# Kernel tuning notes

Hardware: AMD Instinct MI355X
Metric: run time of the kernel (lower is better)

## Reference

```python
import jax, jax.numpy as jnp
import numpy as np

B, P, ENC, EMB, DEC, ATT, V = 64, 196, 512, 512, 512, 512, 10000
CLS_E, NCLS = 512, 200
MAX_LEN = 52
MAX_T = MAX_LEN - 1  # decode steps = max(caption_lengths) - 1


def setup_inputs() -> dict:
    key = jax.random.key(0)
    ks = jax.random.split(key, 24)
    s = 0.02
    u = lambda k, shp: jax.random.uniform(k, shp, jnp.float32, -0.1, 0.1)
    n = lambda k, shp: jax.random.normal(k, shp, jnp.float32) * s
    cap_len = jax.random.randint(ks[2], (B, 1), 2, MAX_LEN + 1)
    cap_len = cap_len.at[0, 0].set(MAX_LEN)  # ensure max decode length is static MAX_T
    return {
        "encoder_out": jax.random.normal(ks[0], (B, P, ENC), jnp.float32),
        "encoded_captions": jax.random.randint(ks[1], (B, MAX_LEN), 0, V),
        "caption_lengths": cap_len,
        "class_k": jax.random.randint(ks[3], (B, 1), 0, NCLS),
        "emb_W": u(ks[4], (V, EMB)),
        "cls_emb_W": u(ks[5], (NCLS, CLS_E)),
        "enc_att_W": n(ks[6], (ENC, ATT)), "enc_att_b": jnp.zeros((ATT,), jnp.float32),
        "dec_att_W": n(ks[7], (DEC, ATT)), "dec_att_b": jnp.zeros((ATT,), jnp.float32),
        "full_att_w": n(ks[8], (ATT,)), "full_att_b": jnp.zeros((), jnp.float32),
        "init_h_W": n(ks[9], (ENC + CLS_E, DEC)), "init_h_b": jnp.zeros((DEC,), jnp.float32),
        "init_c_W": n(ks[10], (ENC + CLS_E, DEC)), "init_c_b": jnp.zeros((DEC,), jnp.float32),
        "f_beta_W": n(ks[11], (DEC, ENC)), "f_beta_b": jnp.zeros((ENC,), jnp.float32),
        "lstm_Wih": n(ks[12], (4 * DEC, EMB + ENC + CLS_E)),
        "lstm_Whh": n(ks[13], (4 * DEC, DEC)),
        "lstm_bih": jnp.zeros((4 * DEC,), jnp.float32),
        "lstm_bhh": jnp.zeros((4 * DEC,), jnp.float32),
        "fc_W": u(ks[14], (DEC, V)), "fc_b": jnp.zeros((V,), jnp.float32),
    }


def reference(encoder_out, encoded_captions, caption_lengths, class_k,
              emb_W, cls_emb_W, enc_att_W, enc_att_b, dec_att_W, dec_att_b,
              full_att_w, full_att_b, init_h_W, init_h_b, init_c_W, init_c_b,
              f_beta_W, f_beta_b, lstm_Wih, lstm_Whh, lstm_bih, lstm_bhh,
              fc_W, fc_b):
    # Sort by descending caption length (torch: caption_lengths.sort(descending=True))
    lens = caption_lengths[:, 0]
    sort_ind = jnp.argsort(-lens)
    lens_s = lens[sort_ind]
    enc = encoder_out[sort_ind]              # [B,P,ENC]
    caps = encoded_captions[sort_ind]        # [B,L]
    embs = emb_W[caps]                       # [B,L,EMB]
    # NOTE: original code does NOT sort class_k -- faithful to that.
    cls_emb = cls_emb_W[class_k[:, 0]]       # [B,CLS_E] (class_embedding[:,0,:])
    dec_len = lens_s - 1                     # decode_lengths

    init_in = jnp.concatenate([enc.mean(axis=1), cls_emb], axis=1)
    h = init_in @ init_h_W + init_h_b        # [B,DEC]
    c = init_in @ init_c_W + init_c_b
    att1 = enc @ enc_att_W + enc_att_b       # [B,P,ATT] (same every step in torch)

    def step(carry, xs):
        h, c = carry
        emb_t, t = xs                        # emb_t: [B,EMB]
        active = (t < dec_len)[:, None]      # ragged batch_size_t truncation as mask
        # attention
        att2 = h @ dec_att_W + dec_att_b
        e = jnp.einsum('bpa,a->bp', jax.nn.relu(att1 + att2[:, None, :]), full_att_w) + full_att_b
        alpha = jax.nn.softmax(e, axis=1)
        awe = jnp.einsum('bpe,bp->be', enc, alpha)
        gate = jax.nn.sigmoid(h @ f_beta_W + f_beta_b)
        awe = gate * awe
        # LSTMCell (torch gate order: i, f, g, o)
        x = jnp.concatenate([emb_t, awe, cls_emb], axis=1)
        gates = x @ lstm_Wih.T + lstm_bih + h @ lstm_Whh.T + lstm_bhh
        i_, f_, g_, o_ = jnp.split(gates, 4, axis=1)
        c_new = jax.nn.sigmoid(f_) * c + jax.nn.sigmoid(i_) * jnp.tanh(g_)
        h_new = jax.nn.sigmoid(o_) * jnp.tanh(c_new)
        # dropout is inference-mode identity
        pred = jnp.where(active, h_new @ fc_W + fc_b, 0.0)
        h = jnp.where(active, h_new, h)
        c = jnp.where(active, c_new, c)
        return (h, c), pred

    xs = (embs[:, :MAX_T].transpose(1, 0, 2), jnp.arange(MAX_T))
    _, preds = jax.lax.scan(step, (h, c), xs)
    predictions = preds.transpose(1, 0, 2)   # [B,MAX_T,V]
    return predictions, caps, dec_len, sort_ind
```

## Files before the change

### kernel.cpp

```cpp
#include <hip/hip_runtime.h>
#include <cstddef>
#include <cstdint>
#include <math.h>

#define BB 64
#define PP 196
#define ENCD 512
#define DECD 512
#define ATTD 512
#define VOC 10000
#define CLSE 512
#define MAXLEN 52
#define MAXT 51
#define G4 2048
#define XDIM 1536

#define OFF_PRED 0
#define OFF_CAPS (BB * MAXT * VOC)
#define OFF_DECLEN (OFF_CAPS + BB * MAXLEN)
#define OFF_SORT (OFF_DECLEN + BB)

static constexpr size_t W_SORT   = 0;
static constexpr size_t W_DECLEN = 64;
static constexpr size_t W_CAPS   = 128;
static constexpr size_t W_CLS    = 3584;
static constexpr size_t W_H      = W_CLS + BB * CLSE;
static constexpr size_t W_C      = W_H + BB * DECD;
static constexpr size_t W_ININ   = W_C + BB * DECD;
static constexpr size_t W_EXCH   = W_ININ + BB * 1024;
static constexpr size_t W_AWE    = W_EXCH + BB * 1024;
static constexpr size_t W_CLSPRE = W_AWE + BB * ENCD;
static constexpr size_t W_W3P    = W_CLSPRE + BB * G4;
static constexpr size_t W_W2P    = W_W3P + (size_t)256 * 8 * 512;
static constexpr size_t W_HALL   = W_W2P + (size_t)256 * 8 * 1024;
static constexpr size_t W_ATT1   = W_HALL + (size_t)BB * MAXT * DECD;
static constexpr size_t W_CNTP   = W_ATT1 + (size_t)BB * PP * ATTD;
static constexpr size_t W_CNTX   = W_CNTP + 3264;
static constexpr size_t W_PAWE   = W_CNTX + 3264;
static constexpr size_t W_CPRE2  = W_PAWE + (size_t)BB * 4 * 520;
static constexpr size_t W_END    = W_CPRE2 + (size_t)MAXT * BB * G4;

__device__ __forceinline__ float sigm(float x) { return 1.f / (1.f + expf(-x)); }

__device__ __forceinline__ double cohLd(const double* p) {
    return __hip_atomic_load(p, __ATOMIC_RELAXED, __HIP_MEMORY_SCOPE_AGENT);
}
__device__ __forceinline__ float cohLdF(const float* p) {
    return __hip_atomic_load(p, __ATOMIC_RELAXED, __HIP_MEMORY_SCOPE_AGENT);
}
__device__ __forceinline__ void cohSt(double* p, double v) {
    __hip_atomic_store(p, v, __ATOMIC_RELAXED, __HIP_MEMORY_SCOPE_AGENT);
}
__device__ __forceinline__ void cohStF(float* p, float v) {
    __hip_atomic_store(p, v, __ATOMIC_RELAXED, __HIP_MEMORY_SCOPE_AGENT);
}

__global__ void setup_kernel(const int* __restrict__ cap_len, float* __restrict__ out,
                             int* __restrict__ sortind, int* __restrict__ declen,
                             int* __restrict__ cnt) {
    __shared__ int sl[BB];
    int i = threadIdx.x;
    for (int k = i; k < 6528; k += 64) cnt[k] = 0;
    sl[i] = cap_len[i];
    __syncthreads();
    int li = sl[i];
    int rank = 0;
    for (int j = 0; j < BB; j++) {
        int lj = sl[j];
        rank += (lj > li) || (lj == li && j < i);
    }
    sortind[rank] = i;
    declen[rank] = li - 1;
    out[OFF_SORT + rank] = (float)i;
    out[OFF_DECLEN + rank] = (float)(li - 1);
}

__global__ void gather_kernel(const int* __restrict__ ecaps, const int* __restrict__ classk,
                              const float* __restrict__ clsW, const int* __restrict__ sortind,
                              int* __restrict__ caps_i, float* __restrict__ cls,
                              float* __restrict__ out) {
    int idx = blockIdx.x * 256 + threadIdx.x;
    if (idx < BB * MAXLEN) {
        int b = idx / MAXLEN, t2 = idx - b * MAXLEN;
        int sb = sortind[b];
        int v = ecaps[sb * MAXLEN + t2];
// ... 175 lines not shown
            float4 b4 = *(const float4*)&Bs[kk][tx * 4];
            float a[4] = {a4.x, a4.y, a4.z, a4.w};
#pragma unroll
            for (int i = 0; i < 4; i++) {
                acc[i][0] = fmaf(a[i], b4.x, acc[i][0]);
                acc[i][1] = fmaf(a[i], b4.y, acc[i][1]);
                acc[i][2] = fmaf(a[i], b4.z, acc[i][2]);
                acc[i][3] = fmaf(a[i], b4.w, acc[i][3]);
            }
        }
    }
#pragma unroll
    for (int i = 0; i < 4; i++) {
        int bl = ty * 4 + i;
        int n = n0 + tx * 4;
        float4 cp = *(const float4*)&clspreg[bl * G4 + n];
        float4 o;
        o.x = acc[i][0] + cp.x; o.y = acc[i][1] + cp.y;
        o.z = acc[i][2] + cp.z; o.w = acc[i][3] + cp.w;
        *(float4*)&cpre2[((size_t)t * 64 + bl) * G4 + n] = o;
    }
}

__global__ __launch_bounds__(256)
void attq_kernel(const float* __restrict__ att1g, const float* __restrict__ encg,
                 const float* __restrict__ hG, const float* __restrict__ Wd,
                 const float* __restrict__ Fb, const float* __restrict__ dab,
                 const float* __restrict__ fbb, const float* __restrict__ fullw,
                 const float* __restrict__ fullb, const int* __restrict__ sortind,
                 const int* __restrict__ declen, float* __restrict__ exch,
                 float* __restrict__ paweG, int* __restrict__ cntX,
                 int* __restrict__ cntP, float* __restrict__ aweG, int t) {
    const int blk = blockIdx.x;
    const int b = blk & 63, q = blk >> 6;
    if (t >= declen[b]) return;
    const int tid = threadIdx.x;
    const int lane = tid & 63, wvid = tid >> 6;

    __shared__ float hS[512];
    __shared__ float pa[256], pb[256];
    __shared__ float att2F[512];
    __shared__ float esS[52];
    __shared__ float redA[1], redB[1];
    __shared__ float pawe[4 * 520];
    __shared__ int finS;

    hS[tid] = hG[b * 512 + tid];
    hS[tid + 256] = hG[b * 512 + 256 + tid];
    __syncthreads();

    {
        const int c = tid & 127, kh = tid >> 7;
        const int col = 128 * q + c;
        const float* wd = Wd + (size_t)(kh << 8) * 512 + col;
        const float* fb = Fb + (size_t)(kh << 8) * 512 + col;
        const float* hp = hS + (kh << 8);
        float a2 = 0.f, fg = 0.f;
#pragma unroll 16
        for (int k = 0; k < 256; k++) {
            float hv = hp[k];
            a2 = fmaf(hv, wd[(size_t)k * 512], a2);
            fg = fmaf(hv, fb[(size_t)k * 512], fg);
        }
        pa[tid] = a2; pb[tid] = fg;
    }
    __syncthreads();
    if (tid < 128) {
        int col = 128 * q + tid;
        cohStF(&exch[b * 1024 + col], pa[tid] + pa[tid + 128] + dab[col]);
        cohStF(&exch[b * 1024 + 512 + col], pb[tid] + pb[tid + 128] + fbb[col]);
    }
    __syncthreads();
    if (tid == 0) {
        int* cx = &cntX[t * 64 + b];
        __hip_atomic_fetch_add(cx, 1, __ATOMIC_RELAXED, __HIP_MEMORY_SCOPE_AGENT);
        while (__hip_atomic_load(cx, __ATOMIC_RELAXED, __HIP_MEMORY_SCOPE_AGENT) < 4)
            __builtin_amdgcn_s_sleep(2);
    }
    __syncthreads();
    att2F[tid] = cohLdF(&exch[b * 1024 + tid]);
    att2F[tid + 256] = cohLdF(&exch[b * 1024 + 256 + tid]);
    __syncthreads();

    const float fbv = fullb[0];
    {
        float4 t0 = *(const float4*)&att2F[lane * 8];
        float4 t1 = *(const float4*)&att2F[lane * 8 + 4];
        float4 w0 = *(const float4*)&fullw[lane * 8];
        float4 w1 = *(const float4*)&fullw[lane * 8 + 4];
        const float* a1b = att1g + (size_t)b * PP * 512;
        for (int lp = wvid; lp < 49; lp += 4) {
            int p = 49 * q + lp;
            const float4* ar = (const float4*)(a1b + (size_t)p * 512) + lane * 2;
            float4 u0 = ar[0], u1 = ar[1];
            float s = fmaxf(u0.x + t0.x, 0.f) * w0.x + fmaxf(u0.y + t0.y, 0.f) * w0.y
                    + fmaxf(u0.z + t0.z, 0.f) * w0.z + fmaxf(u0.w + t0.w, 0.f) * w0.w
                    + fmaxf(u1.x + t1.x, 0.f) * w1.x + fmaxf(u1.y + t1.y, 0.f) * w1.y
                    + fmaxf(u1.z + t1.z, 0.f) * w1.z + fmaxf(u1.w + t1.w, 0.f) * w1.w;
#pragma unroll
            for (int off = 32; off; off >>= 1) s += __shfl_down(s, off, 64);
            if (lane == 0) esS[lp] = s + fbv;
        }
    }
    __syncthreads();
    if (tid < 64) {
        float v = (tid < 49) ? esS[tid] : -1e30f;
#pragma unroll
        for (int off = 32; off; off >>= 1) v = fmaxf(v, __shfl_down(v, off, 64));
        if (tid == 0) redA[0] = v;
    }
    __syncthreads();
    const float mq = redA[0];
    if (tid < 64) {
        float ev = (tid < 49) ? expf(esS[tid] - mq) : 0.f;
        float sv = ev;
#pragma unroll
        for (int off = 32; off; off >>= 1) sv += __shfl_down(sv, off, 64);
        if (tid == 0) redB[0] = sv;
        if (tid < 49) esS[tid] = ev;
    }
    __syncthreads();
    const float Sq = redB[0];

    const int sb = sortind[b];
    {
        float aw[8] = {};
        const float* encb = encg + (size_t)sb * PP * 512 + lane;
        for (int lp = wvid; lp < 49; lp += 4) {
            int p = 49 * q + lp;
            float al = esS[lp];
            const float* ep = encb + (size_t)p * 512;
#pragma unroll
            for (int i = 0; i < 8; i++) aw[i] = fmaf(al, ep[i << 6], aw[i]);
        }
#pragma unroll
        for (int i = 0; i < 8; i++) pawe[wvid * 520 + (i << 6) + lane] = aw[i];
    }
    __syncthreads();
    {
        const int k2 = 2 * tid;
        const int base = ((b << 2) + q) * 520;
        float s0 = pawe[k2] + pawe[520 + k2] + pawe[2 * 520 + k2] + pawe[3 * 520 + k2];
        float s1 = pawe[k2 + 1] + pawe[520 + k2 + 1] + pawe[2 * 520 + k2 + 1] + pawe[3 * 520 + k2 + 1];
        double d;
        *(float2*)&d = make_float2(s0, s1);
        cohSt((double*)&paweG[base + k2], d);
        if (tid == 0) {
            cohStF(&paweG[base + 512], Sq);
            cohStF(&paweG[base + 513], mq);
        }
    }
    __syncthreads();

    if (tid == 0) {
        int prev = __hip_atomic_fetch_add(&cntP[t * 64 + b], 1,
                                          __ATOMIC_RELAXED, __HIP_MEMORY_SCOPE_AGENT);
        finS = (prev == 3);
    }
    __syncthreads();
    if (finS) {
        float mv[4], sv[4];
#pragma unroll
        for (int qq = 0; qq < 4; qq++) {
            mv[qq] = cohLdF(&paweG[((b << 2) + qq) * 520 + 513]);
            sv[qq] = cohLdF(&paweG[((b << 2) + qq) * 520 + 512]);
        }
        float M = fmaxf(fmaxf(mv[0], mv[1]), fmaxf(mv[2], mv[3]));
        float f0 = expf(mv[0] - M), f1 = expf(mv[1] - M);
        float f2 = expf(mv[2] - M), f3 = expf(mv[3] - M);
        float inv = 1.f / (sv[0] * f0 + sv[1] * f1 + sv[2] * f2 + sv[3] * f3);
        const int k2 = 2 * tid;
        const double* pd = (const double*)paweG;
        float a0, a1;
        {
            double d0 = cohLd(pd + ((b << 2) + 0) * 260 + tid);
            double d1 = cohLd(pd + ((b << 2) + 1) * 260 + tid);
            double d2 = cohLd(pd + ((b << 2) + 2) * 260 + tid);
            double d3 = cohLd(pd + ((b << 2) + 3) * 260 + tid);
            float2 g0 = *(float2*)&d0, g1 = *(float2*)&d1;
            float2 g2 = *(float2*)&d2, g3 = *(float2*)&d3;
            a0 = g0.x * f0 + g1.x * f1 + g2.x * f2 + g3.x * f3;
            a1 = g0.y * f0 + g1.y * f1 + g2.y * f2 + g3.y * f3;
        }
        double gpair = cohLd((const double*)&exch[b * 1024 + 512 + k2]);
        float2 g2v = *(float2*)&gpair;
        float2 o = make_float2(a0 * inv * sigm(g2v.x), a1 * inv * sigm(g2v.y));
        *(float2*)&aweG[b * 512 + k2] = o;
    }
}

template<int PRE>
__global__ __launch_bounds__(256)
void gatestep_kernel(const float* __restrict__ embW, const float* __restrict__ W2p,
                     const float* __restrict__ W3p, const float* __restrict__ cpre,
                     const float* __restrict__ aweG, const float* __restrict__ hG,
                     const int* __restrict__ caps_i, const int* __restrict__ declen,
                     float* __restrict__ hOut, float* __restrict__ cG,
                     float* __restrict__ hall, int t) {
    const int j = blockIdx.x, tid = threadIdx.x;
    const int lane = tid & 63, wvid = tid >> 6;
    const int d0 = j * 2;
    const int NCH = PRE ? 8 : 12;
    const int WST = PRE ? 516 : 1028;
    __shared__ float stage[64 * 132];
    __shared__ float W2res[8 * 1028];
    __shared__ float W3res[8 * 516];
    __shared__ float Gs[8 * 66];
    __shared__ float CsS[64 * 8];
    __shared__ int capS[64];
    __shared__ int declen_s[64];

    if (PRE) {
        for (int idx = tid; idx < 1024; idx += 256) {
            int cc = idx >> 7, pos = (idx & 127) << 2;
            *(float4*)&W2res[cc * 516 + pos] =
                *(const float4*)&W2p[(size_t)j * 8192 + cc * 1024 + 512 + pos];
        }
    } else {
        for (int idx = tid; idx < 2048; idx += 256) {
            int cc = idx >> 8, pos = (idx & 255) << 2;
            *(float4*)&W2res[cc * 1028 + pos] =
                *(const float4*)&W2p[(size_t)j * 8192 + cc * 1024 + pos];
        }
    }
    for (int idx = tid; idx < 1024; idx += 256) {
        int cc = idx >> 7, pos = (idx & 127) << 2;
        *(float4*)&W3res[cc * 516 + pos] =
            *(const float4*)&W3p[(size_t)j * 4096 + cc * 512 + pos];
    }
    for (int idx = tid; idx < 512; idx += 256) {
        int r = idx >> 3, cc = idx & 7;
        CsS[idx] = cpre[(r << 11) + ((cc >> 1) << 9) + d0 + (cc & 1)];
    }
    if (tid < 64) {
        if (!PRE) capS[tid] = caps_i[tid * MAXLEN + t];
        declen_s[tid] = declen[tid];
    }

    float ac0 = 0.f, ac1 = 0.f;
    for (int ch = 0; ch < NCH; ch++) {
        __syncthreads();
        {
            const float4* src;
            if (PRE) {
                src = (ch < 4)
                    ? (const float4*)(aweG + ((size_t)lane << 9) + (ch << 7) + (wvid << 5))
                    : (const float4*)(hG + ((size_t)lane << 9) + ((ch - 4) << 7) + (wvid << 5));
            } else {
                if (ch < 4)
                    src = (const float4*)(embW + ((size_t)capS[lane] << 9) + (ch << 7) + (wvid << 5));
                else if (ch < 8)
                    src = (const float4*)(aweG + ((size_t)lane << 9) + ((ch - 4) << 7) + (wvid << 5));
                else
                    src = (const float4*)(hG + ((size_t)lane << 9) + ((ch - 8) << 7) + (wvid << 5));
            }
            float4 tmp[8];
#pragma unroll
            for (int i = 0; i < 8; i++) tmp[i] = src[i];
#pragma unroll
            for (int i = 0; i < 8; i++)
                *(float4*)&stage[lane * 132 + (wvid << 5) + (i << 2)] = tmp[i];
        }
        __syncthreads();
        const float* sp = &stage[lane * 132];
        const int hh0 = PRE ? 4 : 8;
        const float* v0p = (ch < hh0) ? &W2res[wvid * WST + (ch << 7)]
                                      : &W3res[wvid * 516 + ((ch - hh0) << 7)];
        const float* v1p = (ch < hh0) ? &W2res[(wvid + 4) * WST + (ch << 7)]
                                      : &W3res[(wvid + 4) * 516 + ((ch - hh0) << 7)];
#pragma unroll 8
        for (int kk = 0; kk < 128; kk += 4) {
            float4 av = *(const float4*)(sp + kk);
            float4 u0 = *(const float4*)(v0p + kk);
            float4 u1 = *(const float4*)(v1p + kk);
            ac0 = fmaf(av.x, u0.x, fmaf(av.y, u0.y, fmaf(av.z, u0.z, fmaf(av.w, u0.w, ac0))));
            ac1 = fmaf(av.x, u1.x, fmaf(av.y, u1.y, fmaf(av.z, u1.z, fmaf(av.w, u1.w, ac1))));
        }
    }
    Gs[wvid * 66 + lane]       = ac0 + CsS[(lane << 3) + wvid];
    Gs[(wvid + 4) * 66 + lane] = ac1 + CsS[(lane << 3) + wvid + 4];
    __syncthreads();
    if (tid < 128) {
        int r2 = tid & 63, dd = tid >> 6;
        if (t < declen_s[r2]) {
            float iv = Gs[(0 + dd) * 66 + r2];
            float fv = Gs[(2 + dd) * 66 + r2];
            float gv = Gs[(4 + dd) * 66 + r2];
            float ov = Gs[(6 + dd) * 66 + r2];
            float cold = cG[r2 * 512 + d0 + dd];
            float cn = sigm(fv) * cold + sigm(iv) * tanhf(gv);
            float hn = sigm(ov) * tanhf(cn);
            cG[r2 * 512 + d0 + dd] = cn;
            hOut[r2 * 512 + d0 + dd] = hn;
            hall[((size_t)r2 * MAXT + t) * 512 + d0 + dd] = hn;
        }
    }
}

__global__ __launch_bounds__(256)
void fc_kernel(const float* __restrict__ hall, const float* __restrict__ fcW,
               const float* __restrict__ fcb, const int* __restrict__ declen,
               float* __restrict__ out) {
    __shared__ float As[16][68];
    __shared__ float Bs[16][132];
    int tid = threadIdx.x;
    int n0 = blockIdx.x * 128, m0 = blockIdx.y * 64;
    int tx = tid & 15, ty = tid >> 4;
    int lm = tid >> 2, lk4 = (tid & 3) * 4;
    int bkk = tid >> 4, bnn8 = (tid & 15) * 8;
    const float* arow = hall + (size_t)(m0 + lm) * DECD;
    bool nfull = (n0 + 128 <= VOC);
    float acc[4][8] = {};
    for (int k0 = 0; k0 < 512; k0 += 16) {
        float4 av = *(const float4*)(arow + k0 + lk4);
        float4 bv0, bv1;
        const float* bp = fcW + (size_t)(k0 + bkk) * VOC;
        if (nfull) {
            bv0 = *(const float4*)(bp + n0 + bnn8);
            bv1 = *(const float4*)(bp + n0 + bnn8 + 4);
        } else {
            int nb = n0 + bnn8;
            float tv[8];
#pragma unroll
            for (int u = 0; u < 8; u++) tv[u] = (nb + u < VOC) ? bp[nb + u] : 0.f;
            bv0 = make_float4(tv[0], tv[1], tv[2], tv[3]);
            bv1 = make_float4(tv[4], tv[5], tv[6], tv[7]);
        }
        __syncthreads();
        As[lk4 + 0][lm] = av.x; As[lk4 + 1][lm] = av.y;
        As[lk4 + 2][lm] = av.z; As[lk4 + 3][lm] = av.w;
        *(float4*)&Bs[bkk][bnn8] = bv0;
        *(float4*)&Bs[bkk][bnn8 + 4] = bv1;
        __syncthreads();
#pragma unroll
        for (int kk = 0; kk < 16; kk++) {
            float4 a4 = *(const float4*)&As[kk][ty * 4];
            float4 b40 = *(const float4*)&Bs[kk][tx * 8];
            float4 b41 = *(const float4*)&Bs[kk][tx * 8 + 4];
            float a[4] = {a4.x, a4.y, a4.z, a4.w};
#pragma unroll
            for (int i = 0; i < 4; i++) {
                acc[i][0] = fmaf(a[i], b40.x, acc[i][0]);
                acc[i][1] = fmaf(a[i], b40.y, acc[i][1]);
                acc[i][2] = fmaf(a[i], b40.z, acc[i][2]);
                acc[i][3] = fmaf(a[i], b40.w, acc[i][3]);
                acc[i][4] = fmaf(a[i], b41.x, acc[i][4]);
                acc[i][5] = fmaf(a[i], b41.y, acc[i][5]);
                acc[i][6] = fmaf(a[i], b41.z, acc[i][6]);
                acc[i][7] = fmaf(a[i], b41.w, acc[i][7]);
            }
        }
    }
#pragma unroll
    for (int i = 0; i < 4; i++) {
        int m = m0 + ty * 4 + i;
        int b = m / MAXT, tq = m - b * MAXT;
        bool act = tq < declen[b];
        int n = n0 + tx * 8;
        if (nfull) {
            float4 o0, o1;
            o0.x = act ? acc[i][0] + fcb[n + 0] : 0.f;
            o0.y = act ? acc[i][1] + fcb[n + 1] : 0.f;
            o0.z = act ? acc[i][2] + fcb[n + 2] : 0.f;
            o0.w = act ? acc[i][3] + fcb[n + 3] : 0.f;
            o1.x = act ? acc[i][4] + fcb[n + 4] : 0.f;
            o1.y = act ? acc[i][5] + fcb[n + 5] : 0.f;
            o1.z = act ? acc[i][6] + fcb[n + 6] : 0.f;
            o1.w = act ? acc[i][7] + fcb[n + 7] : 0.f;
            *(float4*)(out + (size_t)m * VOC + n) = o0;
            *(float4*)(out + (size_t)m * VOC + n + 4) = o1;
        } else {
#pragma unroll
            for (int jj = 0; jj < 8; jj++) {
                int nn = n + jj;
                if (nn < VOC) out[(size_t)m * VOC + nn] = act ? acc[i][jj] + fcb[nn] : 0.f;
            }
        }
    }
}

extern "C" void kernel_launch(void* const* d_in, const int* in_sizes, int n_in,
                              void* d_out, int out_size, void* d_ws, size_t ws_size,
                              hipStream_t stream) {
    const float* enc     = (const float*)d_in[0];
    const int*   ecaps   = (const int*)d_in[1];
    const int*   lens    = (const int*)d_in[2];
    const int*   classk  = (const int*)d_in[3];
    const float* embW    = (const float*)d_in[4];
    const float* clsW    = (const float*)d_in[5];
    const float* encattW = (const float*)d_in[6];
    const float* encattb = (const float*)d_in[7];
    const float* decattW = (const float*)d_in[8];
    const float* decattb = (const float*)d_in[9];
    const float* fullw   = (const float*)d_in[10];
    const float* fullb   = (const float*)d_in[11];
    const float* ihW     = (const float*)d_in[12];
    const float* ihb     = (const float*)d_in[13];
    const float* icW     = (const float*)d_in[14];
    const float* icb     = (const float*)d_in[15];
    const float* fbW     = (const float*)d_in[16];
    const float* fbb     = (const float*)d_in[17];
    const float* Wih     = (const float*)d_in[18];
    const float* Whh     = (const float*)d_in[19];
    const float* bih     = (const float*)d_in[20];
    const float* bhh     = (const float*)d_in[21];
    const float* fcW     = (const float*)d_in[22];
    const float* fcb     = (const float*)d_in[23];

    float* out = (float*)d_out;
    float* ws  = (float*)d_ws;
    int*   wsi = (int*)d_ws;

    int*   sortind = wsi + W_SORT;
    int*   declen  = wsi + W_DECLEN;
    int*   caps_i  = wsi + W_CAPS;
    float* cls     = ws + W_CLS;
    float* h       = ws + W_H;
    float* c       = ws + W_C;
    float* initin  = ws + W_ININ;
    float* exch    = ws + W_EXCH;
    float* awe     = ws + W_AWE;
    float* clspre  = ws + W_CLSPRE;
    float* W3p     = ws + W_W3P;
    float* W2p     = ws + W_W2P;
    float* hall    = ws + W_HALL;
    float* att1    = ws + W_ATT1;
    int*   cntP    = wsi + W_CNTP;
    int*   cntX    = wsi + W_CNTX;
    float* pawe    = ws + W_PAWE;
    float* cpre2   = ws + W_CPRE2;

    const bool pre = ws_size >= W_END * 4;

    setup_kernel<<<1, 64, 0, stream>>>(lens, out, sortind, declen, cntP);
    gather_kernel<<<141, 256, 0, stream>>>(ecaps, classk, clsW, sortind, caps_i, cls, out);
    mean_cls_kernel<<<BB, 256, 0, stream>>>(enc, cls, sortind, initin);
    init_hc_kernel<<<256, 256, 0, stream>>>(initin, ihW, ihb, icW, icb, h, c);
    pack_w2p_kernel<<<8192, 256, 0, stream>>>(Wih, W2p);
    pack_w3p_kernel<<<4096, 256, 0, stream>>>(Whh, W3p);
    att1_kernel<<<dim3(8, 196), 256, 0, stream>>>(enc, encattW, encattb, sortind, att1);
    clspre_kernel<<<32, 256, 0, stream>>>(cls, Wih, bih, bhh, clspre);
    if (pre)
        embpre_kernel<<<dim3(32, 51), 256, 0, stream>>>(embW, Wih, clspre, caps_i, cpre2);

    for (int t = 0; t < MAXT; t++) {
        attq_kernel<<<256, 256, 0, stream>>>(att1, enc, h, decattW, fbW,
                                             decattb, fbb, fullw, fullb,
                                             sortind, declen, exch, pawe,
                                             cntX, cntP, awe, t);
        if (pre)
            gatestep_kernel<1><<<256, 256, 0, stream>>>(embW, W2p, W3p,
                cpre2 + (size_t)t * 64 * G4, awe, h, caps_i, declen, h, c, hall, t);
        else
            gatestep_kernel<0><<<256, 256, 0, stream>>>(embW, W2p, W3p,
                clspre, awe, h, caps_i, declen, h, c, hall, t);
    }

    fc_kernel<<<dim3(79, 51), 256, 0, stream>>>(hall, fcW, fcb, declen, out);
}
```

Before: 3.720 ms.

## Fuse decode loop into one persistent cooperative kernel with flag-based sync

Replaces the 102 per-step kernel launches (attention plus gate step per timestep) with a single cooperative persistent kernel that loops over all timesteps. Blocks coordinate through global flags for awe readiness and per-block h completion, with h double-buffered. Weight slices stay resident in shared memory across steps, so they are not reloaded every step. The fc kernel's per-thread column mapping is also changed to split into two strided halves. The cost is larger shared memory per block and spin-wait synchronization, with deadlock risk if all 256 blocks cannot be co-resident.

```diff
diff --git a/kernel.cpp b/kernel.cpp
--- a/kernel.cpp
+++ b/kernel.cpp
@@ -1,4 +1,5 @@
 #include <hip/hip_runtime.h>
+#include <hip/hip_cooperative_groups.h>
 #include <cstddef>
 #include <cstdint>
 #include <math.h>
@@ -23,9 +24,14 @@
 static constexpr size_t W_SORT   = 0;
 static constexpr size_t W_DECLEN = 64;
 static constexpr size_t W_CAPS   = 128;
-static constexpr size_t W_CLS    = 3584;
+static constexpr size_t W_CNTP   = 3456;
+static constexpr size_t W_CNTX   = W_CNTP + 3264;
+static constexpr size_t W_AWEF   = W_CNTX + 3264;
+static constexpr size_t W_HFLG   = W_AWEF + 64;
+static constexpr size_t W_CLS    = W_HFLG + 256;
 static constexpr size_t W_H      = W_CLS + BB * CLSE;
-static constexpr size_t W_C      = W_H + BB * DECD;
+static constexpr size_t W_H2     = W_H + BB * DECD;
+static constexpr size_t W_C      = W_H2 + BB * DECD;
 static constexpr size_t W_ININ   = W_C + BB * DECD;
 static constexpr size_t W_EXCH   = W_ININ + BB * 1024;
 static constexpr size_t W_AWE    = W_EXCH + BB * 1024;
@@ -34,9 +40,7 @@
 static constexpr size_t W_W2P    = W_W3P + (size_t)256 * 8 * 512;
 static constexpr size_t W_HALL   = W_W2P + (size_t)256 * 8 * 1024;
 static constexpr size_t W_ATT1   = W_HALL + (size_t)BB * MAXT * DECD;
-static constexpr size_t W_CNTP   = W_ATT1 + (size_t)BB * PP * ATTD;
-static constexpr size_t W_CNTX   = W_CNTP + 3264;
-static constexpr size_t W_PAWE   = W_CNTX + 3264;
+static constexpr size_t W_PAWE   = W_ATT1 + (size_t)BB * PP * ATTD;
 static constexpr size_t W_CPRE2  = W_PAWE + (size_t)BB * 4 * 520;
 static constexpr size_t W_END    = W_CPRE2 + (size_t)MAXT * BB * G4;
 
@@ -48,10 +52,16 @@
 __device__ __forceinline__ float cohLdF(const float* p) {
     return __hip_atomic_load(p, __ATOMIC_RELAXED, __HIP_MEMORY_SCOPE_AGENT);
 }
+__device__ __forceinline__ int cohLdI(const int* p) {
+    return __hip_atomic_load(p, __ATOMIC_RELAXED, __HIP_MEMORY_SCOPE_AGENT);
+}
 __device__ __forceinline__ void cohSt(double* p, double v) {
     __hip_atomic_store(p, v, __ATOMIC_RELAXED, __HIP_MEMORY_SCOPE_AGENT);
 }
 __device__ __forceinline__ void cohStF(float* p, float v) {
+    __hip_atomic_store(p, v, __ATOMIC_RELAXED, __HIP_MEMORY_SCOPE_AGENT);
+}
+__device__ __forceinline__ void cohStI(int* p, int v) {
     __hip_atomic_store(p, v, __ATOMIC_RELAXED, __HIP_MEMORY_SCOPE_AGENT);
 }
 
@@ -60,7 +70,7 @@
                              int* __restrict__ cnt) {
     __shared__ int sl[BB];
     int i = threadIdx.x;
-    for (int k = i; k < 6528; k += 64) cnt[k] = 0;
+    for (int k = i; k < 6848; k += 64) cnt[k] = 0;
     sl[i] = cap_len[i];
     __syncthreads();
     int li = sl[i];
@@ -282,278 +292,376 @@
     }
 }
 
+template<int PRE>
 __global__ __launch_bounds__(256)
-void attq_kernel(const float* __restrict__ att1g, const float* __restrict__ encg,
-                 const float* __restrict__ hG, const float* __restrict__ Wd,
-                 const float* __restrict__ Fb, const float* __restrict__ dab,
-                 const float* __restrict__ fbb, const float* __restrict__ fullw,
-                 const float* __restrict__ fullb, const int* __restrict__ sortind,
-                 const int* __restrict__ declen, float* __restrict__ exch,
-                 float* __restrict__ paweG, int* __restrict__ cntX,
-                 int* __restrict__ cntP, float* __restrict__ aweG, int t) {
-    const int blk = blockIdx.x;
+void loop_kernel(const float* __restrict__ att1g, const float* __restrict__ encg,
+                 const float* __restrict__ embW, const float* __restrict__ W2p,
+                 const float* __restrict__ W3p, const float* __restrict__ cpreg,
+                 const float* __restrict__ Wd, const float* __restrict__ Fb,
+                 const float* __restrict__ dab, const float* __restrict__ fbb,
+                 const float* __restrict__ fullw, const float* __restrict__ fullb,
+                 const int* __restrict__ sortind, const int* __restrict__ declen,
+                 const int* __restrict__ caps_i,
+                 float* __restrict__ h1, float* __restrict__ h2,
+                 const float* __restrict__ c0G, float* __restrict__ hall,
+                 float* __restrict__ exch, float* __restrict__ paweG,
+                 int* __restrict__ cntX, int* __restrict__ cntP,
+                 int* __restrict__ aweflag, int* __restrict__ hflag,
+                 float* __restrict__ aweG) {
+    const int blk = blockIdx.x, tid = threadIdx.x;
+    const int lane = tid & 63, wvid = tid >> 6;
     const int b = blk & 63, q = blk >> 6;
-    if (t >= declen[b]) return;
-    const int tid = threadIdx.x;
-    const int lane = tid & 63, wvid = tid >> 6;
-
+    const int d0 = blk * 2;
+    constexpr int WST = PRE ? 516 : 1028;
+
+    __shared__ float stage[64 * 132];
+    __shared__ float W2res[8 * WST];
+    __shared__ float W3res[8 * 516];
     __shared__ float hS[512];
+    __shared__ float att2F[512];
     __shared__ float pa[256], pb[256];
-    __shared__ float att2F[512];
     __shared__ float esS[52];
     __shared__ float redA[1], redB[1];
     __shared__ float pawe[4 * 520];
-    __shared__ int finS;
-
-    hS[tid] = hG[b * 512 + tid];
-    hS[tid + 256] = hG[b * 512 + 256 + tid];
-    __syncthreads();
-
-    {
-        const int c = tid & 127, kh = tid >> 7;
-        const int col = 128 * q + c;
-        const float* wd = Wd + (size_t)(kh << 8) * 512 + col;
-        const float* fb = Fb + (size_t)(kh << 8) * 512 + col;
-        const float* hp = hS + (kh << 8);
-        float a2 = 0.f, fg = 0.f;
-#pragma unroll 16
-        for (int k = 0; k < 256; k++) {
-            float hv = hp[k];
-            a2 = fmaf(hv, wd[(size_t)k * 512], a2);
-            fg = fmaf(hv, fb[(size_t)k * 512], fg);
-        }
-        pa[tid] = a2; pb[tid] = fg;
-    }
-    __syncthreads();
-    if (tid < 128) {
-        int col = 128 * q + tid;
-        cohStF(&exch[b * 1024 + col], pa[tid] + pa[tid + 128] + dab[col]);
-        cohStF(&exch[b * 1024 + 512 + col], pb[tid] + pb[tid + 128] + fbb[col]);
-    }
-    __syncthreads();
-    if (tid == 0) {
-        int* cx = &cntX[t * 64 + b];
-        __hip_atomic_fetch_add(cx, 1, __ATOMIC_RELAXED, __HIP_MEMORY_SCOPE_AGENT);
-        while (__hip_atomic_load(cx, __ATOMIC_RELAXED, __HIP_MEMORY_SCOPE_AGENT) < 4)
-            __builtin_amdgcn_s_sleep(2);
-    }
-    __syncthreads();
-    att2F[tid] = cohLdF(&exch[b * 1024 + tid]);
-    att2F[tid + 256] = cohLdF(&exch[b * 1024 + 256 + tid]);
-    __syncthreads();
-
-    const float fbv = fullb[0];
-    {
-        float4 t0 = *(const float4*)&att2F[lane * 8];
-        float4 t1 = *(const float4*)&att2F[lane * 8 + 4];
-        float4 w0 = *(const float4*)&fullw[lane * 8];
-        float4 w1 = *(const float4*)&fullw[lane * 8 + 4];
-        const float* a1b = att1g + (size_t)b * PP * 512;
-        for (int lp = wvid; lp < 49; lp += 4) {
-            int p = 49 * q + lp;
-            const float4* ar = (const float4*)(a1b + (size_t)p * 512) + lane * 2;
-            float4 u0 = ar[0], u1 = ar[1];
-            float s = fmaxf(u0.x + t0.x, 0.f) * w0.x + fmaxf(u0.y + t0.y, 0.f) * w0.y
-                    + fmaxf(u0.z + t0.z, 0.f) * w0.z + fmaxf(u0.w + t0.w, 0.f) * w0.w
-                    + fmaxf(u1.x + t1.x, 0.f) * w1.x + fmaxf(u1.y + t1.y, 0.f) * w1.y
-                    + fmaxf(u1.z + t1.z, 0.f) * w1.z + fmaxf(u1.w + t1.w, 0.f) * w1.w;
-#pragma unroll
-            for (int off = 32; off; off >>= 1) s += __shfl_down(s, off, 64);
-            if (lane == 0) esS[lp] = s + fbv;
-        }
-    }
-    __syncthreads();
-    if (tid < 64) {
-        float v = (tid < 49) ? esS[tid] : -1e30f;
-#pragma unroll
-        for (int off = 32; off; off >>= 1) v = fmaxf(v, __shfl_down(v, off, 64));
-        if (tid == 0) redA[0] = v;
-    }
-    __syncthreads();
-    const float mq = redA[0];
-    if (tid < 64) {
-        float ev = (tid < 49) ? expf(esS[tid] - mq) : 0.f;
-        float sv = ev;
-#pragma unroll
-        for (int off = 32; off; off >>= 1) sv += __shfl_down(sv, off, 64);
-        if (tid == 0) redB[0] = sv;
-        if (tid < 49) esS[tid] = ev;
-    }
-    __syncthreads();
-    const float Sq = redB[0];
-
-    const int sb = sortind[b];
-    {
-        float aw[8] = {};
-        const float* encb = encg + (size_t)sb * PP * 512 + lane;
-        for (int lp = wvid; lp < 49; lp += 4) {
-            int p = 49 * q + lp;
-            float al = esS[lp];
-            const float* ep = encb + (size_t)p * 512;
-#pragma unroll
-            for (int i = 0; i < 8; i++) aw[i] = fmaf(al, ep[i << 6], aw[i]);
-        }
-#pragma unroll
-        for (int i = 0; i < 8; i++) pawe[wvid * 520 + (i << 6) + lane] = aw[i];
-    }
-    __syncthreads();
-    {
-        const int k2 = 2 * tid;
-        const int base = ((b << 2) + q) * 520;
-        float s0 = pawe[k2] + pawe[520 + k2] + pawe[2 * 520 + k2] + pawe[3 * 520 + k2];
-        float s1 = pawe[k2 + 1] + pawe[520 + k2 + 1] + pawe[2 * 520 + k2 + 1] + pawe[3 * 520 + k2 + 1];
-        double d;
-        *(float2*)&d = make_float2(s0, s1);
-        cohSt((double*)&paweG[base + k2], d);
-        if (tid == 0) {
-            cohStF(&paweG[base + 512], Sq);
-            cohStF(&paweG[base + 513], mq);
-        }
-    }
-    __syncthreads();
-
-    if (tid == 0) {
-        int prev = __hip_atomic_fetch_add(&cntP[t * 64 + b], 1,
-                                          __ATOMIC_RELAXED, __HIP_MEMORY_SCOPE_AGENT);
-        finS = (prev == 3);
-    }
-    __syncthreads();
-    if (finS) {
-        float mv[4], sv[4];
-#pragma unroll
-        for (int qq = 0; qq < 4; qq++) {
-            mv[qq] = cohLdF(&paweG[((b << 2) + qq) * 520 + 513]);
-            sv[qq] = cohLdF(&paweG[((b << 2) + qq) * 520 + 512]);
-        }
-        float M = fmaxf(fmaxf(mv[0], mv[1]), fmaxf(mv[2], mv[3]));
-        float f0 = expf(mv[0] - M), f1 = expf(mv[1] - M);
-        float f2 = expf(mv[2] - M), f3 = expf(mv[3] - M);
-        float inv = 1.f / (sv[0] * f0 + sv[1] * f1 + sv[2] * f2 + sv[3] * f3);
-        const int k2 = 2 * tid;
-        const double* pd = (const double*)paweG;
-        float a0, a1;
-        {
-            double d0 = cohLd(pd + ((b << 2) + 0) * 260 + tid);
-            double d1 = cohLd(pd + ((b << 2) + 1) * 260 + tid);
-            double d2 = cohLd(pd + ((b << 2) + 2) * 260 + tid);
-            double d3 = cohLd(pd + ((b << 2) + 3) * 260 + tid);
-            float2 g0 = *(float2*)&d0, g1 = *(float2*)&d1;
-            float2 g2 = *(float2*)&d2, g3 = *(float2*)&d3;
-            a0 = g0.x * f0 + g1.x * f1 + g2.x * f2 + g3.x * f3;
-            a1 = g0.y * f0 + g1.y * f1 + g2.y * f2 + g3.y * f3;
-        }
-        double gpair = cohLd((const double*)&exch[b * 1024 + 512 + k2]);
-        float2 g2v = *(float2*)&gpair;
-        float2 o = make_float2(a0 * inv * sigm(g2v.x), a1 * inv * sigm(g2v.y));
-        *(float2*)&aweG[b * 512 + k2] = o;
-    }
-}
-
-template<int PRE>
-__global__ __launch_bounds__(256)
-void gatestep_kernel(const float* __restrict__ embW, const float* __restrict__ W2p,
-                     const float* __restrict__ W3p, const float* __restrict__ cpre,
-                     const float* __restrict__ aweG, const float* __restrict__ hG,
-                     const int* __restrict__ caps_i, const int* __restrict__ declen,
-                     float* __restrict__ hOut, float* __restrict__ cG,
-                     float* __restrict__ hall, int t) {
-    const int j = blockIdx.x, tid = threadIdx.x;
-    const int lane = tid & 63, wvid = tid >> 6;
-    const int d0 = j * 2;
-    const int NCH = PRE ? 8 : 12;
-    const int WST = PRE ? 516 : 1028;
-    __shared__ float stage[64 * 132];
-    __shared__ float W2res[8 * 1028];
-    __shared__ float W3res[8 * 516];
     __shared__ float Gs[8 * 66];
     __shared__ float CsS[64 * 8];
+    __shared__ float cS[64 * 2];
+    __shared__ float hRes[64 * 2];
     __shared__ int capS[64];
     __shared__ int declen_s[64];
+    __shared__ int finS;
 
     if (PRE) {
         for (int idx = tid; idx < 1024; idx += 256) {
             int cc = idx >> 7, pos = (idx & 127) << 2;
             *(float4*)&W2res[cc * 516 + pos] =
-                *(const float4*)&W2p[(size_t)j * 8192 + cc * 1024 + 512 + pos];
+                *(const float4*)&W2p[(size_t)blk * 8192 + cc * 1024 + 512 + pos];
         }
     } else {
         for (int idx = tid; idx < 2048; idx += 256) {
             int cc = idx >> 8, pos = (idx & 255) << 2;
             *(float4*)&W2res[cc * 1028 + pos] =
-                *(const float4*)&W2p[(size_t)j * 8192 + cc * 1024 + pos];
+                *(const float4*)&W2p[(size_t)blk * 8192 + cc * 1024 + pos];
         }
     }
     for (int idx = tid; idx < 1024; idx += 256) {
         int cc = idx >> 7, pos = (idx & 127) << 2;
         *(float4*)&W3res[cc * 516 + pos] =
-            *(const float4*)&W3p[(size_t)j * 4096 + cc * 512 + pos];
-    }
-    for (int idx = tid; idx < 512; idx += 256) {
-        int r = idx >> 3, cc = idx & 7;
-        CsS[idx] = cpre[(r << 11) + ((cc >> 1) << 9) + d0 + (cc & 1)];
-    }
-    if (tid < 64) {
-        if (!PRE) capS[tid] = caps_i[tid * MAXLEN + t];
-        declen_s[tid] = declen[tid];
-    }
-
-    float ac0 = 0.f, ac1 = 0.f;
-    for (int ch = 0; ch < NCH; ch++) {
-        __syncthreads();
+            *(const float4*)&W3p[(size_t)blk * 4096 + cc * 512 + pos];
+    }
+    if (!PRE) {
+        for (int idx = tid; idx < 512; idx += 256) {
+            int r = idx >> 3, cc = idx & 7;
+            CsS[idx] = cpreg[(r << 11) + ((cc >> 1) << 9) + d0 + (cc & 1)];
+        }
+    }
+    if (tid < 128) {
+        int r = tid & 63, dd = tid >> 6;
+        cS[r * 2 + dd] = c0G[r * 512 + d0 + dd];
+        hRes[r * 2 + dd] = h1[r * 512 + d0 + dd];
+    }
+    if (tid < 64) declen_s[tid] = declen[tid];
+    const int sb = sortind[b];
+    __syncthreads();
+    const int dlb = declen_s[b];
+
+    for (int t = 0; t < MAXT; t++) {
+        const float* hcur = (t & 1) ? h2 : h1;
+        float* hnxt = (t & 1) ? h1 : h2;
+
+        if (t < dlb) {
+            {
+                double hv = cohLd((const double*)&hcur[b * 512 + 2 * tid]);
+                *(double*)&hS[2 * tid] = hv;
+            }
+            __syncthreads();
+            {
+                const int c = tid & 127, kh = tid >> 7;
+                const int col = 128 * q + c;
+                const float* wd = Wd + (size_t)(kh << 8) * 512 + col;
+                const float* fb = Fb + (size_t)(kh << 8) * 512 + col;
+                const float* hp = hS + (kh << 8);
+                float a2 = 0.f, fg = 0.f;
+#pragma unroll 16
+                for (int k = 0; k < 256; k++) {
+                    float hv = hp[k];
+                    a2 = fmaf(hv, wd[(size_t)k * 512], a2);
+                    fg = fmaf(hv, fb[(size_t)k * 512], fg);
+                }
+                pa[tid] = a2; pb[tid] = fg;
+            }
+            __syncthreads();
+            if (tid < 128) {
+                int col = 128 * q + tid;
+                cohStF(&exch[b * 1024 + col], pa[tid] + pa[tid + 128] + dab[col]);
+                cohStF(&exch[b * 1024 + 512 + col], pb[tid] + pb[tid + 128] + fbb[col]);
+            }
+            __syncthreads();
+            if (tid == 0) {
+                int* cx = &cntX[t * 64 + b];
+                __hip_atomic_fetch_add(cx, 1, __ATOMIC_RELAXED, __HIP_MEMORY_SCOPE_AGENT);
+                while (__hip_atomic_load(cx, __ATOMIC_RELAXED, __HIP_MEMORY_SCOPE_AGENT) < 4)
+                    __builtin_amdgcn_s_sleep(2);
+            }
+            __syncthreads();
+            att2F[tid] = cohLdF(&exch[b * 1024 + tid]);
+            att2F[tid + 256] = cohLdF(&exch[b * 1024 + 256 + tid]);
+            __syncthreads();
+
+            const float fbv = fullb[0];
+            {
+                float4 t0 = *(const float4*)&att2F[lane * 8];
+                float4 t1 = *(const float4*)&att2F[lane * 8 + 4];
+                float4 w0 = *(const float4*)&fullw[lane * 8];
+                float4 w1 = *(const float4*)&fullw[lane * 8 + 4];
+                const float* a1b = att1g + (size_t)b * PP * 512;
+                for (int lp = wvid; lp < 49; lp += 4) {
+                    int p = 49 * q + lp;
+                    const float4* ar = (const float4*)(a1b + (size_t)p * 512) + lane * 2;
+                    float4 u0 = ar[0], u1 = ar[1];
+                    float s = fmaxf(u0.x + t0.x, 0.f) * w0.x + fmaxf(u0.y + t0.y, 0.f) * w0.y
+                            + fmaxf(u0.z + t0.z, 0.f) * w0.z + fmaxf(u0.w + t0.w, 0.f) * w0.w
+                            + fmaxf(u1.x + t1.x, 0.f) * w1.x + fmaxf(u1.y + t1.y, 0.f) * w1.y
+                            + fmaxf(u1.z + t1.z, 0.f) * w1.z + fmaxf(u1.w + t1.w, 0.f) * w1.w;
+#pragma unroll
+                    for (int off = 32; off; off >>= 1) s += __shfl_down(s, off, 64);
+                    if (lane == 0) esS[lp] = s + fbv;
+                }
+            }
+            __syncthreads();
+            if (tid < 64) {
+                float v = (tid < 49) ? esS[tid] : -1e30f;
+#pragma unroll
+                for (int off = 32; off; off >>= 1) v = fmaxf(v, __shfl_down(v, off, 64));
+                if (tid == 0) redA[0] = v;
+            }
+            __syncthreads();
+            const float mq = redA[0];
+            if (tid < 64) {
+                float ev = (tid < 49) ? expf(esS[tid] - mq) : 0.f;
+                float sv = ev;
+#pragma unroll
+                for (int off = 32; off; off >>= 1) sv += __shfl_down(sv, off, 64);
+                if (tid == 0) redB[0] = sv;
+                if (tid < 49) esS[tid] = ev;
+            }
+            __syncthreads();
+            const float Sq = redB[0];
+            {
+                float aw[8] = {};
+                const float* encb = encg + (size_t)sb * PP * 512 + lane;
+                for (int lp = wvid; lp < 49; lp += 4) {
+                    int p = 49 * q + lp;
+                    float al = esS[lp];
+                    const float* ep = encb + (size_t)p * 512;
+#pragma unroll
+                    for (int i = 0; i < 8; i++) aw[i] = fmaf(al, ep[i << 6], aw[i]);
+                }
+#pragma unroll
+                for (int i = 0; i < 8; i++) pawe[wvid * 520 + (i << 6) + lane] = aw[i];
+            }
+            __syncthreads();
+            {
+                const int k2 = 2 * tid;
+                const int base = ((b << 2) + q) * 520;
+                float s0 = pawe[k2] + pawe[520 + k2] + pawe[2 * 520 + k2] + pawe[3 * 520 + k2];
+                float s1 = pawe[k2 + 1] + pawe[520 + k2 + 1] + pawe[2 * 520 + k2 + 1] + pawe[3 * 520 + k2 + 1];
+                double d;
+                *(float2*)&d = make_float2(s0, s1);
+                cohSt((double*)&paweG[base + k2], d);
+                if (tid == 0) {
+                    cohStF(&paweG[base + 512], Sq);
+                    cohStF(&paweG[base + 513], mq);
+                }
+            }
+            __syncthreads();
+            if (tid == 0) {
+                int prev = __hip_atomic_fetch_add(&cntP[t * 64 + b], 1,
+                                                  __ATOMIC_RELAXED, __HIP_MEMORY_SCOPE_AGENT);
+                finS = (prev == 3);
+            }
+            __syncthreads();
+            if (finS) {
+                float mv[4], sv[4];
+#pragma unroll
+                for (int qq = 0; qq < 4; qq++) {
+                    mv[qq] = cohLdF(&paweG[((b << 2) + qq) * 520 + 513]);
+                    sv[qq] = cohLdF(&paweG[((b << 2) + qq) * 520 + 512]);
+                }
+                float M = fmaxf(fmaxf(mv[0], mv[1]), fmaxf(mv[2], mv[3]));
+                float f0 = expf(mv[0] - M), f1 = expf(mv[1] - M);
+                float f2 = expf(mv[2] - M), f3 = expf(mv[3] - M);
+                float inv = 1.f / (sv[0] * f0 + sv[1] * f1 + sv[2] * f2 + sv[3] * f3);
+                const int k2 = 2 * tid;
+                const double* pd = (const double*)paweG;
+                float a0, a1;
+                {
+                    double dv0 = cohLd(pd + ((b << 2) + 0) * 260 + tid);
+                    double dv1 = cohLd(pd + ((b << 2) + 1) * 260 + tid);
+                    double dv2 = cohLd(pd + ((b << 2) + 2) * 260 + tid);
+                    double dv3 = cohLd(pd + ((b << 2) + 3) * 260 + tid);
+                    float2 g0 = *(float2*)&dv0, g1 = *(float2*)&dv1;
+                    float2 g2 = *(float2*)&dv2, g3 = *(float2*)&dv3;
+                    a0 = g0.x * f0 + g1.x * f1 + g2.x * f2 + g3.x * f3;
+                    a1 = g0.y * f0 + g1.y * f1 + g2.y * f2 + g3.y * f3;
+                }
+                double gpair = cohLd((const double*)&exch[b * 1024 + 512 + k2]);
+                float2 g2v = *(float2*)&gpair;
+                double st;
+                *(float2*)&st = make_float2(a0 * inv * sigm(g2v.x), a1 * inv * sigm(g2v.y));
+                cohSt((double*)&aweG[b * 512 + k2], st);
+            }
+            __syncthreads();
+            if (finS && tid == 0) cohStI(&aweflag[b], t + 1);
+        }
+
+        if (PRE) {
+            const float* cp = cpreg + (size_t)t * 64 * G4;
+            for (int idx = tid; idx < 512; idx += 256) {
+                int r = idx >> 3, cc = idx & 7;
+                CsS[idx] = cp[(r << 11) + ((cc >> 1) << 9) + d0 + (cc & 1)];
+            }
+        } else if (tid < 64) {
+            capS[tid] = caps_i[tid * MAXLEN + t];
+        }
+
+        float ac0 = 0.f, ac1 = 0.f;
+
+        if (!PRE) {
+            __syncthreads();
+            for (int ch = 0; ch < 4; ch++) {
+                __syncthreads();
+                {
+                    const float4* src = (const float4*)(embW + ((size_t)capS[lane] << 9) + (ch << 7) + (wvid << 5));
+                    float4 tmp[8];
+#pragma unroll
+                    for (int i = 0; i < 8; i++) tmp[i] = src[i];
+#pragma unroll
+                    for (int i = 0; i < 8; i++)
+                        *(float4*)&stage[lane * 132 + (wvid << 5) + (i << 2)] = tmp[i];
+                }
+                __syncthreads();
+                const float* sp = &stage[lane * 132];
+                const float* v0p = &W2res[wvid * WST + (ch << 7)];
+                const float* v1p = &W2res[(wvid + 4) * WST + (ch << 7)];
+#pragma unroll 8
+                for (int kk = 0; kk < 128; kk += 4) {
+                    float4 av = *(const float4*)(sp + kk);
+                    float4 u0 = *(const float4*)(v0p + kk);
+                    float4 u1 = *(const float4*)(v1p + kk);
+                    ac0 = fmaf(av.x, u0.x, fmaf(av.y, u0.y, fmaf(av.z, u0.z, fmaf(av.w, u0.w, ac0))));
+                    ac1 = fmaf(av.x, u1.x, fmaf(av.y, u1.y, fmaf(av.z, u1.z, fmaf(av.w, u1.w, ac1))));
+                }
+            }
+        }
+
         {
-            const float4* src;
-            if (PRE) {
-                src = (ch < 4)
-                    ? (const float4*)(aweG + ((size_t)lane << 9) + (ch << 7) + (wvid << 5))
-                    : (const float4*)(hG + ((size_t)lane << 9) + ((ch - 4) << 7) + (wvid << 5));
-            } else {
-                if (ch < 4)
-                    src = (const float4*)(embW + ((size_t)capS[lane] << 9) + (ch << 7) + (wvid << 5));
-                else if (ch < 8)
-                    src = (const float4*)(aweG + ((size_t)lane << 9) + ((ch - 4) << 7) + (wvid << 5));
-                else
-                    src = (const float4*)(hG + ((size_t)lane << 9) + ((ch - 8) << 7) + (wvid << 5));
-            }
-            float4 tmp[8];
-#pragma unroll
-            for (int i = 0; i < 8; i++) tmp[i] = src[i];
-#pragma unroll
-            for (int i = 0; i < 8; i++)
-                *(float4*)&stage[lane * 132 + (wvid << 5) + (i << 2)] = tmp[i];
-        }
-        __syncthreads();
-        const float* sp = &stage[lane * 132];
-        const int hh0 = PRE ? 4 : 8;
-        const float* v0p = (ch < hh0) ? &W2res[wvid * WST + (ch << 7)]
-                                      : &W3res[wvid * 516 + ((ch - hh0) << 7)];
-        const float* v1p = (ch < hh0) ? &W2res[(wvid + 4) * WST + (ch << 7)]
-                                      : &W3res[(wvid + 4) * 516 + ((ch - hh0) << 7)];
+            double tmp[16];
+            {
+                const double* ap = (const double*)(hcur + ((size_t)lane << 9) + (wvid << 5));
+#pragma unroll
+                for (int i = 0; i < 16; i++) tmp[i] = cohLd(ap + i);
+            }
+            for (int ch = 0; ch < 4; ch++) {
+                __syncthreads();
+#pragma unroll
+                for (int i = 0; i < 8; i++) {
+                    float2 fa = *(float2*)&tmp[2 * i], fb2 = *(float2*)&tmp[2 * i + 1];
+                    *(float4*)&stage[lane * 132 + (wvid << 5) + (i << 2)] =
+                        make_float4(fa.x, fa.y, fb2.x, fb2.y);
+                }
+                __syncthreads();
+                if (ch < 3) {
+                    const double* ap = (const double*)(hcur + ((size_t)lane << 9) + ((ch + 1) << 7) + (wvid << 5));
+#pragma unroll
+                    for (int i = 0; i < 16; i++) tmp[i] = cohLd(ap + i);
+                }
+                const float* sp = &stage[lane * 132];
+                const float* v0p = &W3res[wvid * 516 + (ch << 7)];
+                const float* v1p = &W3res[(wvid + 4) * 516 + (ch << 7)];
 #pragma unroll 8
-        for (int kk = 0; kk < 128; kk += 4) {
-            float4 av = *(const float4*)(sp + kk);
-            float4 u0 = *(const float4*)(v0p + kk);
-            float4 u1 = *(const float4*)(v1p + kk);
-            ac0 = fmaf(av.x, u0.x, fmaf(av.y, u0.y, fmaf(av.z, u0.z, fmaf(av.w, u0.w, ac0))));
-            ac1 = fmaf(av.x, u1.x, fmaf(av.y, u1.y, fmaf(av.z, u1.z, fmaf(av.w, u1.w, ac1))));
-        }
-    }
-    Gs[wvid * 66 + lane]       = ac0 + CsS[(lane << 3) + wvid];
-    Gs[(wvid + 4) * 66 + lane] = ac1 + CsS[(lane << 3) + wvid + 4];
-    __syncthreads();
-    if (tid < 128) {
-        int r2 = tid & 63, dd = tid >> 6;
-        if (t < declen_s[r2]) {
-            float iv = Gs[(0 + dd) * 66 + r2];
-            float fv = Gs[(2 + dd) * 66 + r2];
-            float gv = Gs[(4 + dd) * 66 + r2];
-            float ov = Gs[(6 + dd) * 66 + r2];
-            float cold = cG[r2 * 512 + d0 + dd];
-            float cn = sigm(fv) * cold + sigm(iv) * tanhf(gv);
-            float hn = sigm(ov) * tanhf(cn);
-            cG[r2 * 512 + d0 + dd] = cn;
-            hOut[r2 * 512 + d0 + dd] = hn;
-            hall[((size_t)r2 * MAXT + t) * 512 + d0 + dd] = hn;
-        }
+                for (int kk = 0; kk < 128; kk += 4) {
+                    float4 av = *(const float4*)(sp + kk);
+                    float4 u0 = *(const float4*)(v0p + kk);
+                    float4 u1 = *(const float4*)(v1p + kk);
+                    ac0 = fmaf(av.x, u0.x, fmaf(av.y, u0.y, fmaf(av.z, u0.z, fmaf(av.w, u0.w, ac0))));
+                    ac1 = fmaf(av.x, u1.x, fmaf(av.y, u1.y, fmaf(av.z, u1.z, fmaf(av.w, u1.w, ac1))));
+                }
+            }
+        }
+
+        if (tid < 64) {
+            while (!(t >= declen_s[tid] || cohLdI(&aweflag[tid]) > t))
+                __builtin_amdgcn_s_sleep(2);
+        }
+        __syncthreads();
+
+        {
+            double tmp[16];
+            {
+                const double* ap = (const double*)(aweG + ((size_t)lane << 9) + (wvid << 5));
+#pragma unroll
+                for (int i = 0; i < 16; i++) tmp[i] = cohLd(ap + i);
+            }
+            for (int ch = 0; ch < 4; ch++) {
+                __syncthreads();
+#pragma unroll
+                for (int i = 0; i < 8; i++) {
+                    float2 fa = *(float2*)&tmp[2 * i], fb2 = *(float2*)&tmp[2 * i + 1];
+                    *(float4*)&stage[lane * 132 + (wvid << 5) + (i << 2)] =
+                        make_float4(fa.x, fa.y, fb2.x, fb2.y);
+                }
+                __syncthreads();
+                if (ch < 3) {
+                    const double* ap = (const double*)(aweG + ((size_t)lane << 9) + ((ch + 1) << 7) + (wvid << 5));
+#pragma unroll
+                    for (int i = 0; i < 16; i++) tmp[i] = cohLd(ap + i);
+                }
+                const float* sp = &stage[lane * 132];
+                const int off = PRE ? (ch << 7) : (512 + (ch << 7));
+                const float* v0p = &W2res[wvid * WST + off];
+                const float* v1p = &W2res[(wvid + 4) * WST + off];
+#pragma unroll 8
+                for (int kk = 0; kk < 128; kk += 4) {
+                    float4 av = *(const float4*)(sp + kk);
+                    float4 u0 = *(const float4*)(v0p + kk);
+                    float4 u1 = *(const float4*)(v1p + kk);
+                    ac0 = fmaf(av.x, u0.x, fmaf(av.y, u0.y, fmaf(av.z, u0.z, fmaf(av.w, u0.w, ac0))));
+                    ac1 = fmaf(av.x, u1.x, fmaf(av.y, u1.y, fmaf(av.z, u1.z, fmaf(av.w, u1.w, ac1))));
+                }
+            }
+        }
+
+        Gs[wvid * 66 + lane]       = ac0 + CsS[(lane << 3) + wvid];
+        Gs[(wvid + 4) * 66 + lane] = ac1 + CsS[(lane << 3) + wvid + 4];
+        __syncthreads();
+        if (tid < 128) {
+            int r2 = tid & 63, dd = tid >> 6;
+            if (t < declen_s[r2]) {
+                float iv = Gs[(0 + dd) * 66 + r2];
+                float fv = Gs[(2 + dd) * 66 + r2];
+                float gv = Gs[(4 + dd) * 66 + r2];
+                float ov = Gs[(6 + dd) * 66 + r2];
+                float cold = cS[r2 * 2 + dd];
+                float cn = sigm(fv) * cold + sigm(iv) * tanhf(gv);
+                float hn = sigm(ov) * tanhf(cn);
+                cS[r2 * 2 + dd] = cn;
+                hRes[r2 * 2 + dd] = hn;
+            }
+        }
+        __syncthreads();
+        if (tid < 64) {
+            double hv2 = *(double*)&hRes[tid * 2];
+            cohSt((double*)&hnxt[tid * 512 + d0], hv2);
+            if (t < declen_s[tid])
+                *(double*)&hall[((size_t)tid * MAXT + t) * 512 + d0] = hv2;
+        }
+        __syncthreads();
+        if (tid == 0) cohStI(&hflag[blk], t + 1);
+
+        while (cohLdI(&hflag[tid]) <= t)
+            __builtin_amdgcn_s_sleep(2);
+        __syncthreads();
     }
 }
 
@@ -595,8 +703,8 @@
 #pragma unroll
         for (int kk = 0; kk < 16; kk++) {
             float4 a4 = *(const float4*)&As[kk][ty * 4];
-            float4 b40 = *(const float4*)&Bs[kk][tx * 8];
-            float4 b41 = *(const float4*)&Bs[kk][tx * 8 + 4];
+            float4 b40 = *(const float4*)&Bs[kk][tx * 4];
+            float4 b41 = *(const float4*)&Bs[kk][64 + tx * 4];
             float a[4] = {a4.x, a4.y, a4.z, a4.w};
 #pragma unroll
             for (int i = 0; i < 4; i++) {
@@ -614,26 +722,31 @@
 #pragma unroll
     for (int i = 0; i < 4; i++) {
         int m = m0 + ty * 4 + i;
-        int b = m / MAXT, tq = m - b * MAXT;
-        bool act = tq < declen[b];
-        int n = n0 + tx * 8;
+        int bq = m / MAXT, tq = m - bq * MAXT;
+        bool act = tq < declen[bq];
+        int nlo = n0 + tx * 4, nhi = n0 + 64 + tx * 4;
         if (nfull) {
             float4 o0, o1;
-            o0.x = act ? acc[i][0] + fcb[n + 0] : 0.f;
-            o0.y = act ? acc[i][1] + fcb[n + 1] : 0.f;
-            o0.z = act ? acc[i][2] + fcb[n + 2] : 0.f;
-            o0.w = act ? acc[i][3] + fcb[n + 3] : 0.f;
-            o1.x = act ? acc[i][4] + fcb[n + 4] : 0.f;
-            o1.y = act ? acc[i][5] + fcb[n + 5] : 0.f;
-            o1.z = act ? acc[i][6] + fcb[n + 6] : 0.f;
-            o1.w = act ? acc[i][7] + fcb[n + 7] : 0.f;
-            *(float4*)(out + (size_t)m * VOC + n) = o0;
-            *(float4*)(out + (size_t)m * VOC + n + 4) = o1;
+            o0.x = act ? acc[i][0] + fcb[nlo + 0] : 0.f;
+            o0.y = act ? acc[i][1] + fcb[nlo + 1] : 0.f;
+            o0.z = act ? acc[i][2] + fcb[nlo + 2] : 0.f;
+            o0.w = act ? acc[i][3] + fcb[nlo + 3] : 0.f;
+            o1.x = act ? acc[i][4] + fcb[nhi + 0] : 0.f;
+            o1.y = act ? acc[i][5] + fcb[nhi + 1] : 0.f;
+            o1.z = act ? acc[i][6] + fcb[nhi + 2] : 0.f;
+            o1.w = act ? acc[i][7] + fcb[nhi + 3] : 0.f;
+            *(float4*)(out + (size_t)m * VOC + nlo) = o0;
+            *(float4*)(out + (size_t)m * VOC + nhi) = o1;
         } else {
 #pragma unroll
-            for (int jj = 0; jj < 8; jj++) {
-                int nn = n + jj;
+            for (int jj = 0; jj < 4; jj++) {
+                int nn = nlo + jj;
                 if (nn < VOC) out[(size_t)m * VOC + nn] = act ? acc[i][jj] + fcb[nn] : 0.f;
+            }
+#pragma unroll
+            for (int jj = 0; jj < 4; jj++) {
+                int nn = nhi + jj;
+                if (nn < VOC) out[(size_t)m * VOC + nn] = act ? acc[i][4 + jj] + fcb[nn] : 0.f;
             }
         }
     }
@@ -674,8 +787,13 @@
     int*   sortind = wsi + W_SORT;
     int*   declen  = wsi + W_DECLEN;
     int*   caps_i  = wsi + W_CAPS;
+    int*   cntP    = wsi + W_CNTP;
+    int*   cntX    = wsi + W_CNTX;
+    int*   aweflag = wsi + W_AWEF;
+    int*   hflag   = wsi + W_HFLG;
     float* cls     = ws + W_CLS;
-    float* h       = ws + W_H;
+    float* h1      = ws + W_H;
+    float* h2      = ws + W_H2;
     float* c       = ws + W_C;
     float* initin  = ws + W_ININ;
     float* exch    = ws + W_EXCH;
@@ -685,8 +803,6 @@
     float* W2p     = ws + W_W2P;
     float* hall    = ws + W_HALL;
     float* att1    = ws + W_ATT1;
-    int*   cntP    = wsi + W_CNTP;
-    int*   cntX    = wsi + W_CNTX;
     float* pawe    = ws + W_PAWE;
     float* cpre2   = ws + W_CPRE2;
 
@@ -695,7 +811,7 @@
     setup_kernel<<<1, 64, 0, stream>>>(lens, out, sortind, declen, cntP);
     gather_kernel<<<141, 256, 0, stream>>>(ecaps, classk, clsW, sortind, caps_i, cls, out);
     mean_cls_kernel<<<BB, 256, 0, stream>>>(enc, cls, sortind, initin);
-    init_hc_kernel<<<256, 256, 0, stream>>>(initin, ihW, ihb, icW, icb, h, c);
+    init_hc_kernel<<<256, 256, 0, stream>>>(initin, ihW, ihb, icW, icb, h1, c);
     pack_w2p_kernel<<<8192, 256, 0, stream>>>(Wih, W2p);
     pack_w3p_kernel<<<4096, 256, 0, stream>>>(Whh, W3p);
     att1_kernel<<<dim3(8, 196), 256, 0, stream>>>(enc, encattW, encattb, sortind, att1);
@@ -703,18 +819,17 @@
     if (pre)
         embpre_kernel<<<dim3(32, 51), 256, 0, stream>>>(embW, Wih, clspre, caps_i, cpre2);
 
-    for (int t = 0; t < MAXT; t++) {
-        attq_kernel<<<256, 256, 0, stream>>>(att1, enc, h, decattW, fbW,
-                                             decattb, fbb, fullw, fullb,
-                                             sortind, declen, exch, pawe,
-                                             cntX, cntP, awe, t);
-        if (pre)
-            gatestep_kernel<1><<<256, 256, 0, stream>>>(embW, W2p, W3p,
-                cpre2 + (size_t)t * 64 * G4, awe, h, caps_i, declen, h, c, hall, t);
-        else
-            gatestep_kernel<0><<<256, 256, 0, stream>>>(embW, W2p, W3p,
-                clspre, awe, h, caps_i, declen, h, c, hall, t);
-    }
+    const float* cpreArg = pre ? cpre2 : clspre;
+    void* kargs[] = {
+        (void*)&att1, (void*)&enc, (void*)&embW, (void*)&W2p, (void*)&W3p,
+        (void*)&cpreArg, (void*)&decattW, (void*)&fbW, (void*)&decattb, (void*)&fbb,
+        (void*)&fullw, (void*)&fullb, (void*)&sortind, (void*)&declen, (void*)&caps_i,
+        (void*)&h1, (void*)&h2, (void*)&c, (void*)&hall, (void*)&exch, (void*)&pawe,
+        (void*)&cntX, (void*)&cntP, (void*)&aweflag, (void*)&hflag, (void*)&awe
+    };
+    hipLaunchCooperativeKernel(pre ? (const void*)loop_kernel<1>
+                                   : (const void*)loop_kernel<0>,
+                               dim3(256), dim3(256), kargs, 0, stream);
 
     fc_kernel<<<dim3(79, 51), 256, 0, stream>>>(hall, fcW, fcb, declen, out);
 }
```

Result: slower. 4.415 ms (+18.7%).
